# Kernel optimization log

Measured on AMD Instinct MI355X. Metric: run time of the kernel, lower is better.

The kernel has to match this reference:

```python
import jax, jax.numpy as jnp
import numpy as np

B = 131072      # batch size
ORDER = 8       # number of TT modes
N = 64          # grid points per mode (dims[i])
R = 32          # internal TT rank
EPS = 1e-8      # stability_eps
INIT_SCALE = 0.01


def setup_inputs() -> dict:
    key = jax.random.key(0)
    k_idx, k0, kmid, klast = jax.random.split(key, 4)
    indices = jax.random.randint(k_idx, (B, ORDER), 0, N, dtype=jnp.int64)
    # TT cores: core0 (1, N, R), middle cores (ORDER-2, R, N, R), core_last (R, N, 1)
    core0 = jax.random.normal(k0, (1, N, R), dtype=jnp.float32) * INIT_SCALE
    cores_mid = jax.random.normal(kmid, (ORDER - 2, R, N, R), dtype=jnp.float32) * INIT_SCALE
    core_last = jax.random.normal(klast, (R, N, 1), dtype=jnp.float32) * INIT_SCALE
    return {"indices": indices, "core0": core0, "cores_mid": cores_mid, "core_last": core_last}


def _tt_forward(indices, core0, cores_mid, core_last):
    order = 2 + cores_mid.shape[0]
    dims = jnp.array([core0.shape[1]] + [cores_mid.shape[2]] * cores_mid.shape[0]
                     + [core_last.shape[1]], dtype=indices.dtype)
    idx = jnp.clip(indices, 0, dims[None, :] - 1)

    # i == 0: core0[:, idx, :] -> [1, B, R] -> squeeze leading rank-1 -> [B, R]
    v = core0[0, idx[:, 0], :]

    def step(v, core, col_idx):
        sl = core[:, col_idx, :]                                  # [R, B, R']
        norm = jnp.linalg.norm(v, axis=1, keepdims=True) + EPS    # [B, 1]
        v_new = jnp.einsum('br,rbs->bs', v / norm, sl) * norm     # [B, R']
        return v_new

    # middle cores share shape -> scan over them (gather + normalized matvec chain)
    def scan_body(v, inputs):
        core, col = inputs
        return step(v, core, col), None

    mid_cols = idx[:, 1:order - 1].T  # [ORDER-2, B]
    v, _ = jax.lax.scan(scan_body, v, (cores_mid, mid_cols))

    # last core -> [B, 1] -> squeeze -> [B]
    v = step(v, core_last, idx[:, order - 1])
    return v[:, 0]


def reference(indices, core0, cores_mid, core_last):
    return _tt_forward(indices, core0, cores_mid, core_last)
```

## Files before the change

kernel.cpp:

```cpp
#include <hip/hip_runtime.h>
#include <hip/hip_fp16.h>


#define B_TOTAL 131072
#define NDIM 64
#define RANK 32
#define S_BLK 256
#define THREADS 256
#define VSTRIDE_H 40

typedef _Float16 half8 __attribute__((ext_vector_type(8)));
typedef _Float16 half4 __attribute__((ext_vector_type(4)));
typedef float    f32x4 __attribute__((ext_vector_type(4)));

__global__ __launch_bounds__(256) void build_tables(
    const float* __restrict__ core0, const float* __restrict__ mid,
    const float* __restrict__ lastc,
    half8* __restrict__ PKB, __half* __restrict__ T01, float* __restrict__ TL)
{
    const int id = blockIdx.x * 256 + threadIdx.x;
    if (id < 32768) {
        const int l  = id & 63;
        const int f  = (id >> 6) & 1;
        const int c  = (id >> 7) & 63;
        const int tt = id >> 13;
        const int q = l >> 4, li = l & 15;
        const int n = f * 16 + li;
        const int t = 1 + tt;
        half8 h;
        #pragma unroll
        for (int j = 0; j < 8; ++j) {
            const int k = q * 8 + j;
            h[j] = (_Float16)(16.0f * mid[((t * 32 + k) * 64 + c) * 32 + n]);
        }
        PKB[id] = h;
    } else if (id < 163840) {
        const int i2 = id - 32768;
        const int s = i2 & 31, c1 = (i2 >> 5) & 63, c0 = i2 >> 11;
        float acc = 0.f;
        #pragma unroll
        for (int r = 0; r < 32; ++r)
            acc = fmaf(core0[c0 * 32 + r], mid[(r * 64 + c1) * 32 + s], acc);
        T01[(c0 * 64 + c1) * 32 + s] = __float2half(acc * 256.0f);
    } else {
        const int i3 = id - 163840;
        const int c7 = i3 & 63, c6 = (i3 >> 6) & 63, r = i3 >> 12;
        const float* m5 = mid + 5 * 65536;
        float acc = 0.f;
        #pragma unroll
        for (int s = 0; s < 32; ++s)
            acc = fmaf(m5[(r * 64 + c6) * 32 + s], lastc[s * 64 + c7], acc);
        TL[(c6 * 64 + c7) * 32 + r] = acc * 256.0f;
    }
}

__global__ __launch_bounds__(256) void tt_main_t(
    const int* __restrict__ idx, const __half* __restrict__ T01,
    const half8* __restrict__ PKB, const float* __restrict__ TL,
    float* __restrict__ out)
{
    __shared__ __align__(16) __half vbuf[S_BLK * VSTRIDE_H];
    __shared__ unsigned short ord[4][S_BLK];
    __shared__ unsigned char  cols[S_BLK][8];
    __shared__ unsigned int   bases[4][65];
    __shared__ unsigned int   hist[4][64];

    const int tid  = threadIdx.x;
    const int lane = tid & 63;
    const int wv   = tid >> 6;
    const int li   = lane & 15;
    const int quad = lane >> 4;
    const int b0   = blockIdx.x * S_BLK;

    #pragma unroll
    for (int k = 0; k < S_BLK * 8; k += THREADS) {
        const int lin = k + tid;
        int v = idx[b0 * 8 + lin];
        v = min(max(v, 0), NDIM - 1);
        cols[lin >> 3][lin & 7] = (unsigned char)v;
    }
    hist[tid >> 6][tid & 63] = 0;
    __syncthreads();

    unsigned int key[4], rank[4];
    #pragma unroll
    for (int tt = 0; tt < 4; ++tt) {
        key[tt]  = cols[tid][2 + tt];
        rank[tt] = atomicAdd(&hist[tt][key[tt]], 1u);
    }
    __syncthreads();
    {
        const unsigned int v = hist[wv][lane];
        unsigned int inc = v;
        #pragma unroll
        for (int d = 1; d < 64; d <<= 1) {
            const unsigned int n = __shfl_up(inc, d);
            if (lane >= d) inc += n;
        }
        bases[wv][lane] = inc - v;
        if (lane == 63) bases[wv][64] = inc;
    }
    __syncthreads();
    #pragma unroll
    for (int tt = 0; tt < 4; ++tt)
        ord[tt][bases[tt][key[tt]] + rank[tt]] = (unsigned short)tid;
    __syncthreads();

    {
        const int g = tid & 7, gid = tid >> 3;
        #pragma unroll
        for (int it = 0; it < S_BLK / 32; ++it) {
            const int s = it * 32 + gid;
            const int c0 = cols[s][0], c1 = cols[s][1];
            const uint2 q = *reinterpret_cast<const uint2*>(
                T01 + (c0 * 64 + c1) * 32 + 4 * g);
            unsigned int* vp = reinterpret_cast<unsigned int*>(vbuf) + s * (VSTRIDE_H / 2);
            vp[2 * g]     = q.x;
            vp[2 * g + 1] = q.y;
        }
    }
    __syncthreads();

    for (int tt = 0; tt < 4; ++tt) {
        const int cbase = wv * 16;
        half8 A0 = PKB[((tt * 64 + cbase) * 2 + 0) * 64 + lane];
        half8 A1 = PKB[((tt * 64 + cbase) * 2 + 1) * 64 + lane];
        for (int ci = 0; ci < 16; ++ci) {
            const int c = cbase + ci;
            half8 nA0 = A0, nA1 = A1;
            if (ci < 15) {
                nA0 = PKB[((tt * 64 + c + 1) * 2 + 0) * 64 + lane];
                nA1 = PKB[((tt * 64 + c + 1) * 2 + 1) * 64 + lane];
            }
            const int start = (int)bases[tt][c];
            const int end   = (int)bases[tt][c + 1];
            for (int p = start; p < end; p += 16) {
                const int pos = min(p + li, end - 1);
                const int sm  = (int)ord[tt][pos];
                const half8 Bv = *reinterpret_cast<const half8*>(
                    reinterpret_cast<const char*>(vbuf) + sm * 80 + quad * 16);
                f32x4 d0 = {0.f, 0.f, 0.f, 0.f}, d1 = {0.f, 0.f, 0.f, 0.f};
                d0 = __builtin_amdgcn_mfma_f32_16x16x32_f16(A0, Bv, d0, 0, 0, 0);
                d1 = __builtin_amdgcn_mfma_f32_16x16x32_f16(A1, Bv, d1, 0, 0, 0);
                half4 w0, w1;
                #pragma unroll
                for (int r = 0; r < 4; ++r) {
                    w0[r] = (_Float16)d0[r];
                    w1[r] = (_Float16)d1[r];
                }
                char* base = reinterpret_cast<char*>(vbuf) + sm * 80 + quad * 8;
                *reinterpret_cast<half4*>(base)      = w0;
                *reinterpret_cast<half4*>(base + 32) = w1;
            }
            A0 = nA0; A1 = nA1;
        }
        __syncthreads();
    }

    {
        const int g = tid & 7, gid = tid >> 3;
        #pragma unroll
        for (int it = 0; it < S_BLK / 32; ++it) {
            const int s = it * 32 + gid;
            const int c6 = cols[s][6], c7 = cols[s][7];
            const unsigned int* vp =
                reinterpret_cast<const unsigned int*>(vbuf) + s * (VSTRIDE_H / 2);
            const __half2 v01 = *reinterpret_cast<const __half2*>(&vp[2 * g]);
            const __half2 v23 = *reinterpret_cast<const __half2*>(&vp[2 * g + 1]);
            const float4 L = *reinterpret_cast<const float4*>(
                TL + (c6 * 64 + c7) * 32 + 4 * g);
            float o = 0.f;
            o = fmaf(__low2float(v01),  L.x, o);
            o = fmaf(__high2float(v01), L.y, o);
            o = fmaf(__low2float(v23),  L.z, o);
            o = fmaf(__high2float(v23), L.w, o);
            o += __shfl_xor(o, 1);
            o += __shfl_xor(o, 2);
            o += __shfl_xor(o, 4);
            if (g == 0) out[b0 + s] = o * 2.3283064365386963e-10f;
        }
    }
}

#define PKB_OFF 0u
#define TL_OFF  524288u
#define T01_OFF 1048576u

extern "C" void kernel_launch(void* const* d_in, const int* in_sizes, int n_in,
                              void* d_out, int out_size, void* d_ws, size_t ws_size,
                              hipStream_t stream) {
    const int*   idx   = (const int*)d_in[0];
    const float* core0 = (const float*)d_in[1];
    const float* mid   = (const float*)d_in[2];
    const float* lastc = (const float*)d_in[3];
    float* out = (float*)d_out;

    half8*  PKB = (half8*)((char*)d_ws + PKB_OFF);
    float*  TL  = (float*)((char*)d_ws + TL_OFF);
    __half* T01 = (__half*)((char*)d_ws + T01_OFF);

    hipLaunchKernelGGL(build_tables, dim3(294912 / 256), dim3(256), 0, stream,
                       core0, mid, lastc, PKB, T01, TL);
    hipLaunchKernelGGL(tt_main_t, dim3(B_TOTAL / S_BLK), dim3(THREADS), 0, stream,
                       idx, T01, PKB, TL, out);
}
```

Measured before the change: 84.21 us.

## Load-balance MFMA batches across waves via shared descriptor list with prefetch

```diff
diff --git a/kernel.cpp b/kernel.cpp
--- a/kernel.cpp
+++ b/kernel.cpp
@@ -8,6 +8,7 @@
 #define S_BLK 256
 #define THREADS 256
 #define VSTRIDE_H 40
+#define MAXB 80
 
 typedef _Float16 half8 __attribute__((ext_vector_type(8)));
 typedef _Float16 half4 __attribute__((ext_vector_type(4)));
@@ -54,7 +55,7 @@
     }
 }
 
-__global__ __launch_bounds__(256) void tt_main_t(
+__global__ __launch_bounds__(256) void tt_main_p(
     const int* __restrict__ idx, const __half* __restrict__ T01,
     const half8* __restrict__ PKB, const float* __restrict__ TL,
     float* __restrict__ out)
@@ -64,6 +65,8 @@
     __shared__ unsigned char  cols[S_BLK][8];
     __shared__ unsigned int   bases[4][65];
     __shared__ unsigned int   hist[4][64];
+    __shared__ unsigned int   desc[4][MAXB];
+    __shared__ unsigned int   nb[4];
 
     const int tid  = threadIdx.x;
     const int lane = tid & 63;
@@ -80,6 +83,7 @@
         cols[lin >> 3][lin & 7] = (unsigned char)v;
     }
     hist[tid >> 6][tid & 63] = 0;
+    if (tid < 4) nb[tid] = 0;
     __syncthreads();
 
     unsigned int key[4], rank[4];
@@ -104,6 +108,15 @@
     #pragma unroll
     for (int tt = 0; tt < 4; ++tt)
         ord[tt][bases[tt][key[tt]] + rank[tt]] = (unsigned short)tid;
+    {
+        const int tts = tid >> 6, c = tid & 63;
+        const int st = (int)bases[tts][c], en = (int)bases[tts][c + 1];
+        for (int p = st; p < en; p += 16) {
+            const unsigned int ln = (unsigned int)min(16, en - p);
+            const unsigned int slot = atomicAdd(&nb[tts], 1u);
+            desc[tts][slot] = (unsigned int)c | ((unsigned int)p << 6) | (ln << 15);
+        }
+    }
     __syncthreads();
 
     {
@@ -122,37 +135,47 @@
     __syncthreads();
 
     for (int tt = 0; tt < 4; ++tt) {
-        const int cbase = wv * 16;
-        half8 A0 = PKB[((tt * 64 + cbase) * 2 + 0) * 64 + lane];
-        half8 A1 = PKB[((tt * 64 + cbase) * 2 + 1) * 64 + lane];
-        for (int ci = 0; ci < 16; ++ci) {
-            const int c = cbase + ci;
-            half8 nA0 = A0, nA1 = A1;
-            if (ci < 15) {
-                nA0 = PKB[((tt * 64 + c + 1) * 2 + 0) * 64 + lane];
-                nA1 = PKB[((tt * 64 + c + 1) * 2 + 1) * 64 + lane];
+        const int n = (int)nb[tt];
+        int i = wv;
+        int sm = 0;
+        half8 A0 = {0,0,0,0,0,0,0,0}, A1 = {0,0,0,0,0,0,0,0};
+        half8 Bv = {0,0,0,0,0,0,0,0};
+        if (i < n) {
+            const unsigned int d = desc[tt][i];
+            const int c = d & 63, st = (d >> 6) & 511, ln = (d >> 15) & 31;
+            sm = (int)ord[tt][min(st + li, st + ln - 1)];
+            A0 = PKB[((tt * 64 + c) * 2 + 0) * 64 + lane];
+            A1 = PKB[((tt * 64 + c) * 2 + 1) * 64 + lane];
+            Bv = *reinterpret_cast<const half8*>(
+                reinterpret_cast<const char*>(vbuf) + sm * 80 + quad * 16);
+        }
+        while (i < n) {
+            const int inx = i + 4;
+            int smn = 0;
+            half8 A0n = {0,0,0,0,0,0,0,0}, A1n = {0,0,0,0,0,0,0,0};
+            half8 Bvn = {0,0,0,0,0,0,0,0};
+            if (inx < n) {
+                const unsigned int d = desc[tt][inx];
+                const int c = d & 63, st = (d >> 6) & 511, ln = (d >> 15) & 31;
+                smn = (int)ord[tt][min(st + li, st + ln - 1)];
+                A0n = PKB[((tt * 64 + c) * 2 + 0) * 64 + lane];
+                A1n = PKB[((tt * 64 + c) * 2 + 1) * 64 + lane];
+                Bvn = *reinterpret_cast<const half8*>(
+                    reinterpret_cast<const char*>(vbuf) + smn * 80 + quad * 16);
             }
-            const int start = (int)bases[tt][c];
-            const int end   = (int)bases[tt][c + 1];
-            for (int p = start; p < end; p += 16) {
-                const int pos = min(p + li, end - 1);
-                const int sm  = (int)ord[tt][pos];
-                const half8 Bv = *reinterpret_cast<const half8*>(
-                    reinterpret_cast<const char*>(vbuf) + sm * 80 + quad * 16);
-                f32x4 d0 = {0.f, 0.f, 0.f, 0.f}, d1 = {0.f, 0.f, 0.f, 0.f};
-                d0 = __builtin_amdgcn_mfma_f32_16x16x32_f16(A0, Bv, d0, 0, 0, 0);
-                d1 = __builtin_amdgcn_mfma_f32_16x16x32_f16(A1, Bv, d1, 0, 0, 0);
-                half4 w0, w1;
-                #pragma unroll
-                for (int r = 0; r < 4; ++r) {
-                    w0[r] = (_Float16)d0[r];
-                    w1[r] = (_Float16)d1[r];
-                }
-                char* base = reinterpret_cast<char*>(vbuf) + sm * 80 + quad * 8;
-                *reinterpret_cast<half4*>(base)      = w0;
-                *reinterpret_cast<half4*>(base + 32) = w1;
+            f32x4 d0 = {0.f, 0.f, 0.f, 0.f}, d1 = {0.f, 0.f, 0.f, 0.f};
+            d0 = __builtin_amdgcn_mfma_f32_16x16x32_f16(A0, Bv, d0, 0, 0, 0);
+            d1 = __builtin_amdgcn_mfma_f32_16x16x32_f16(A1, Bv, d1, 0, 0, 0);
+            half4 w0, w1;
+            #pragma unroll
+            for (int r = 0; r < 4; ++r) {
+                w0[r] = (_Float16)d0[r];
+                w1[r] = (_Float16)d1[r];
             }
-            A0 = nA0; A1 = nA1;
+            char* base = reinterpret_cast<char*>(vbuf) + sm * 80 + quad * 8;
+            *reinterpret_cast<half4*>(base)      = w0;
+            *reinterpret_cast<half4*>(base + 32) = w1;
+            i = inx; sm = smn; A0 = A0n; A1 = A1n; Bv = Bvn;
         }
         __syncthreads();
     }
@@ -201,6 +224,6 @@
 
     hipLaunchKernelGGL(build_tables, dim3(294912 / 256), dim3(256), 0, stream,
                        core0, mid, lastc, PKB, T01, TL);
-    hipLaunchKernelGGL(tt_main_t, dim3(B_TOTAL / S_BLK), dim3(THREADS), 0, stream,
+    hipLaunchKernelGGL(tt_main_p, dim3(B_TOTAL / S_BLK), dim3(THREADS), 0, stream,
                        idx, T01, PKB, TL, out);
 }
```

Measured after the change: 93.27 us. +10.8%, slower.

## Store vectors in sorted order with ping-pong buffers and software-pipelined column groups

Applied to the files above, without the earlier changes.

```diff
diff --git a/kernel.cpp b/kernel.cpp
--- a/kernel.cpp
+++ b/kernel.cpp
@@ -4,10 +4,9 @@
 
 #define B_TOTAL 131072
 #define NDIM 64
-#define RANK 32
 #define S_BLK 256
 #define THREADS 256
-#define VSTRIDE_H 40
+#define VSH 40
 
 typedef _Float16 half8 __attribute__((ext_vector_type(8)));
 typedef _Float16 half4 __attribute__((ext_vector_type(4)));
@@ -54,16 +53,17 @@
     }
 }
 
-__global__ __launch_bounds__(256) void tt_main_t(
+__global__ __launch_bounds__(256) void tt_main_s(
     const int* __restrict__ idx, const __half* __restrict__ T01,
     const half8* __restrict__ PKB, const float* __restrict__ TL,
     float* __restrict__ out)
 {
-    __shared__ __align__(16) __half vbuf[S_BLK * VSTRIDE_H];
-    __shared__ unsigned short ord[4][S_BLK];
+    __shared__ __align__(16) __half vbuf2[2][S_BLK * VSH];
     __shared__ unsigned char  cols[S_BLK][8];
     __shared__ unsigned int   bases[4][65];
     __shared__ unsigned int   hist[4][64];
+    __shared__ unsigned short nxt[4][S_BLK];
+    __shared__ unsigned short pos0[S_BLK];
 
     const int tid  = threadIdx.x;
     const int lane = tid & 63;
@@ -101,9 +101,15 @@
         if (lane == 63) bases[wv][64] = inc;
     }
     __syncthreads();
-    #pragma unroll
-    for (int tt = 0; tt < 4; ++tt)
-        ord[tt][bases[tt][key[tt]] + rank[tt]] = (unsigned short)tid;
+    {
+        unsigned int p[4];
+        #pragma unroll
+        for (int tt = 0; tt < 4; ++tt) p[tt] = bases[tt][key[tt]] + rank[tt];
+        pos0[tid] = (unsigned short)p[0];
+        #pragma unroll
+        for (int tt = 0; tt < 3; ++tt) nxt[tt][p[tt]] = (unsigned short)p[tt + 1];
+        nxt[3][p[3]] = (unsigned short)tid;
+    }
     __syncthreads();
 
     {
@@ -114,7 +120,8 @@
             const int c0 = cols[s][0], c1 = cols[s][1];
             const uint2 q = *reinterpret_cast<const uint2*>(
                 T01 + (c0 * 64 + c1) * 32 + 4 * g);
-            unsigned int* vp = reinterpret_cast<unsigned int*>(vbuf) + s * (VSTRIDE_H / 2);
+            const int ps = (int)pos0[s];
+            unsigned int* vp = reinterpret_cast<unsigned int*>(&vbuf2[0][ps * VSH]);
             vp[2 * g]     = q.x;
             vp[2 * g + 1] = q.y;
         }
@@ -122,37 +129,73 @@
     __syncthreads();
 
     for (int tt = 0; tt < 4; ++tt) {
+        const __half* src = vbuf2[tt & 1];
+        __half*       dst = vbuf2[(tt + 1) & 1];
         const int cbase = wv * 16;
-        half8 A0 = PKB[((tt * 64 + cbase) * 2 + 0) * 64 + lane];
-        half8 A1 = PKB[((tt * 64 + cbase) * 2 + 1) * 64 + lane];
+        const int bval = (int)bases[tt][cbase + (lane < 17 ? lane : 16)];
+
+        int   stp[2], enp[2], wpp[2];
+        half8 Afp[2][2], Bvp[2];
+        #pragma unroll
+        for (int j = 0; j < 2; ++j) {
+            const int st = __shfl(bval, j);
+            const int en = __shfl(bval, j + 1);
+            const int c  = cbase + j;
+            stp[j] = st; enp[j] = en;
+            Afp[j][0] = PKB[((tt * 64 + c) * 2 + 0) * 64 + lane];
+            Afp[j][1] = PKB[((tt * 64 + c) * 2 + 1) * 64 + lane];
+            int pp = min(st + li, max(en - 1, st)); pp = min(pp, S_BLK - 1);
+            wpp[j] = (int)nxt[tt][pp];
+            Bvp[j] = *reinterpret_cast<const half8*>(&src[pp * VSH + quad * 8]);
+        }
+        #pragma unroll
         for (int ci = 0; ci < 16; ++ci) {
-            const int c = cbase + ci;
-            half8 nA0 = A0, nA1 = A1;
-            if (ci < 15) {
-                nA0 = PKB[((tt * 64 + c + 1) * 2 + 0) * 64 + lane];
-                nA1 = PKB[((tt * 64 + c + 1) * 2 + 1) * 64 + lane];
-            }
-            const int start = (int)bases[tt][c];
-            const int end   = (int)bases[tt][c + 1];
-            for (int p = start; p < end; p += 16) {
-                const int pos = min(p + li, end - 1);
-                const int sm  = (int)ord[tt][pos];
-                const half8 Bv = *reinterpret_cast<const half8*>(
-                    reinterpret_cast<const char*>(vbuf) + sm * 80 + quad * 16);
+            const int cur = ci & 1;
+            const int st = stp[cur], en = enp[cur];
+            if (st < en) {
                 f32x4 d0 = {0.f, 0.f, 0.f, 0.f}, d1 = {0.f, 0.f, 0.f, 0.f};
-                d0 = __builtin_amdgcn_mfma_f32_16x16x32_f16(A0, Bv, d0, 0, 0, 0);
-                d1 = __builtin_amdgcn_mfma_f32_16x16x32_f16(A1, Bv, d1, 0, 0, 0);
+                d0 = __builtin_amdgcn_mfma_f32_16x16x32_f16(Afp[cur][0], Bvp[cur], d0, 0, 0, 0);
+                d1 = __builtin_amdgcn_mfma_f32_16x16x32_f16(Afp[cur][1], Bvp[cur], d1, 0, 0, 0);
                 half4 w0, w1;
                 #pragma unroll
                 for (int r = 0; r < 4; ++r) {
                     w0[r] = (_Float16)d0[r];
                     w1[r] = (_Float16)d1[r];
                 }
-                char* base = reinterpret_cast<char*>(vbuf) + sm * 80 + quad * 8;
+                __half* base = &dst[wpp[cur] * VSH + quad * 4];
                 *reinterpret_cast<half4*>(base)      = w0;
-                *reinterpret_cast<half4*>(base + 32) = w1;
+                *reinterpret_cast<half4*>(base + 16) = w1;
+                for (int p = st + 16; p < en; p += 16) {
+                    const int pp2 = min(p + li, en - 1);
+                    const half8 Bx = *reinterpret_cast<const half8*>(
+                        &src[pp2 * VSH + quad * 8]);
+                    const int wx = (int)nxt[tt][pp2];
+                    f32x4 e0 = {0.f, 0.f, 0.f, 0.f}, e1 = {0.f, 0.f, 0.f, 0.f};
+                    e0 = __builtin_amdgcn_mfma_f32_16x16x32_f16(Afp[cur][0], Bx, e0, 0, 0, 0);
+                    e1 = __builtin_amdgcn_mfma_f32_16x16x32_f16(Afp[cur][1], Bx, e1, 0, 0, 0);
+                    half4 x0, x1;
+                    #pragma unroll
+                    for (int r = 0; r < 4; ++r) {
+                        x0[r] = (_Float16)e0[r];
+                        x1[r] = (_Float16)e1[r];
+                    }
+                    __half* bb = &dst[wx * VSH + quad * 4];
+                    *reinterpret_cast<half4*>(bb)      = x0;
+                    *reinterpret_cast<half4*>(bb + 16) = x1;
+                }
             }
-            A0 = nA0; A1 = nA1;
+            if (ci + 2 < 16) {
+                const int j  = ci + 2;
+                const int st2 = __shfl(bval, j);
+                const int en2 = __shfl(bval, j + 1);
+                const int c2  = cbase + j;
+                stp[cur] = st2; enp[cur] = en2;
+                Afp[cur][0] = PKB[((tt * 64 + c2) * 2 + 0) * 64 + lane];
+                Afp[cur][1] = PKB[((tt * 64 + c2) * 2 + 1) * 64 + lane];
+                int pp = min(st2 + li, max(en2 - 1, st2)); pp = min(pp, S_BLK - 1);
+                wpp[cur] = (int)nxt[tt][pp];
+                Bvp[cur] = *reinterpret_cast<const half8*>(&src[pp * VSH + quad * 8]);
+            }
         }
         __syncthreads();
     }
@@ -164,7 +207,7 @@
             const int s = it * 32 + gid;
             const int c6 = cols[s][6], c7 = cols[s][7];
             const unsigned int* vp =
-                reinterpret_cast<const unsigned int*>(vbuf) + s * (VSTRIDE_H / 2);
+                reinterpret_cast<const unsigned int*>(&vbuf2[0][s * VSH]);
             const __half2 v01 = *reinterpret_cast<const __half2*>(&vp[2 * g]);
             const __half2 v23 = *reinterpret_cast<const __half2*>(&vp[2 * g + 1]);
             const float4 L = *reinterpret_cast<const float4*>(
@@ -201,6 +244,6 @@
 
     hipLaunchKernelGGL(build_tables, dim3(294912 / 256), dim3(256), 0, stream,
                        core0, mid, lastc, PKB, T01, TL);
-    hipLaunchKernelGGL(tt_main_t, dim3(B_TOTAL / S_BLK), dim3(THREADS), 0, stream,
+    hipLaunchKernelGGL(tt_main_s, dim3(B_TOTAL / S_BLK), dim3(THREADS), 0, stream,
                        idx, T01, PKB, TL, out);
 }
```

Result: no change. 83.95 us (-0.3%).

## Template main kernel on block size and launch 1024-sample blocks

Applied to the files above, without the earlier changes.

```diff
diff --git a/kernel.cpp b/kernel.cpp
--- a/kernel.cpp
+++ b/kernel.cpp
@@ -4,10 +4,6 @@
 
 #define B_TOTAL 131072
 #define NDIM 64
-#define RANK 32
-#define S_BLK 256
-#define THREADS 256
-#define VSTRIDE_H 40
 
 typedef _Float16 half8 __attribute__((ext_vector_type(8)));
 typedef _Float16 half4 __attribute__((ext_vector_type(4)));
@@ -54,67 +50,74 @@
     }
 }
 
-__global__ __launch_bounds__(256) void tt_main_t(
+template<int SBLK>
+__global__ __launch_bounds__(SBLK) void tt_main_v(
     const int* __restrict__ idx, const __half* __restrict__ T01,
     const half8* __restrict__ PKB, const float* __restrict__ TL,
     float* __restrict__ out)
 {
-    __shared__ __align__(16) __half vbuf[S_BLK * VSTRIDE_H];
-    __shared__ unsigned short ord[4][S_BLK];
-    __shared__ unsigned char  cols[S_BLK][8];
-    __shared__ unsigned int   bases[4][65];
-    __shared__ unsigned int   hist[4][64];
+    constexpr int NW  = SBLK / 64;
+    constexpr int CPW = 64 / NW;
+    extern __shared__ __align__(16) char smem[];
+    __half*         vbuf  = reinterpret_cast<__half*>(smem);
+    unsigned short* ord   = reinterpret_cast<unsigned short*>(smem + SBLK * 80);
+    unsigned int*   cols2 = reinterpret_cast<unsigned int*>(smem + SBLK * 88);
+    unsigned int*   hist  = reinterpret_cast<unsigned int*>(smem + SBLK * 92);
+    unsigned int*   bases = hist + 256;
 
     const int tid  = threadIdx.x;
     const int lane = tid & 63;
     const int wv   = tid >> 6;
     const int li   = lane & 15;
     const int quad = lane >> 4;
-    const int b0   = blockIdx.x * S_BLK;
-
+    const int b0   = blockIdx.x * SBLK;
+
+    const int4* idx4 = reinterpret_cast<const int4*>(idx) + (size_t)(b0 + tid) * 2;
+    const int4 ia = idx4[0], ib = idx4[1];
+    const int c0 = min(max(ia.x, 0), 63), c1 = min(max(ia.y, 0), 63);
+    int key[4];
+    key[0] = min(max(ia.z, 0), 63);
+    key[1] = min(max(ia.w, 0), 63);
+    key[2] = min(max(ib.x, 0), 63);
+    key[3] = min(max(ib.y, 0), 63);
+    const int c6 = min(max(ib.z, 0), 63), c7 = min(max(ib.w, 0), 63);
+    cols2[tid] = (unsigned)c0 | ((unsigned)c1 << 8) |
+                 ((unsigned)c6 << 16) | ((unsigned)c7 << 24);
+    if (tid < 256) hist[tid] = 0;
+    __syncthreads();
+
+    unsigned int rank[4];
     #pragma unroll
-    for (int k = 0; k < S_BLK * 8; k += THREADS) {
-        const int lin = k + tid;
-        int v = idx[b0 * 8 + lin];
-        v = min(max(v, 0), NDIM - 1);
-        cols[lin >> 3][lin & 7] = (unsigned char)v;
-    }
-    hist[tid >> 6][tid & 63] = 0;
-    __syncthreads();
-
-    unsigned int key[4], rank[4];
-    #pragma unroll
-    for (int tt = 0; tt < 4; ++tt) {
-        key[tt]  = cols[tid][2 + tt];
-        rank[tt] = atomicAdd(&hist[tt][key[tt]], 1u);
-    }
-    __syncthreads();
-    {
-        const unsigned int v = hist[wv][lane];
+    for (int tt = 0; tt < 4; ++tt)
+        rank[tt] = atomicAdd(&hist[tt * 64 + key[tt]], 1u);
+    __syncthreads();
+    if (wv < 4) {
+        const unsigned int v = hist[wv * 64 + lane];
         unsigned int inc = v;
         #pragma unroll
         for (int d = 1; d < 64; d <<= 1) {
             const unsigned int n = __shfl_up(inc, d);
             if (lane >= d) inc += n;
         }
-        bases[wv][lane] = inc - v;
-        if (lane == 63) bases[wv][64] = inc;
+        bases[wv * 65 + lane] = inc - v;
+        if (lane == 63) bases[wv * 65 + 64] = inc;
     }
     __syncthreads();
     #pragma unroll
     for (int tt = 0; tt < 4; ++tt)
-        ord[tt][bases[tt][key[tt]] + rank[tt]] = (unsigned short)tid;
-    __syncthreads();
-
+        ord[tt * SBLK + bases[tt * 65 + key[tt]] + rank[tt]] = (unsigned short)tid;
+
+    __syncthreads();
     {
         const int g = tid & 7, gid = tid >> 3;
         #pragma unroll
-        for (int it = 0; it < S_BLK / 32; ++it) {
-            const int s = it * 32 + gid;
-            const int c0 = cols[s][0], c1 = cols[s][1];
+        for (int it = 0; it < 8; ++it) {
+            const int s = it * (SBLK / 8) + gid;
+            const unsigned cc = cols2[s];
+            const int a = cc & 255, b = (cc >> 8) & 255;
             const uint2 q = *reinterpret_cast<const uint2*>(
-                T01 + (c0 * 64 + c1) * 32 + 4 * g);
-            unsigned int* vp = reinterpret_cast<unsigned int*>(vbuf) + s * (VSTRIDE_H / 2);
+                T01 + (a * 64 + b) * 32 + 4 * g);
+            unsigned int* vp = reinterpret_cast<unsigned int*>(vbuf + s * 40);
             vp[2 * g]     = q.x;
             vp[2 * g + 1] = q.y;
         }
@@ -122,23 +125,22 @@
     __syncthreads();
 
     for (int tt = 0; tt < 4; ++tt) {
-        const int cbase = wv * 16;
+        const int cbase = wv * CPW;
         half8 A0 = PKB[((tt * 64 + cbase) * 2 + 0) * 64 + lane];
         half8 A1 = PKB[((tt * 64 + cbase) * 2 + 1) * 64 + lane];
-        for (int ci = 0; ci < 16; ++ci) {
+        for (int ci = 0; ci < CPW; ++ci) {
             const int c = cbase + ci;
             half8 nA0 = A0, nA1 = A1;
-            if (ci < 15) {
+            if (ci + 1 < CPW) {
                 nA0 = PKB[((tt * 64 + c + 1) * 2 + 0) * 64 + lane];
                 nA1 = PKB[((tt * 64 + c + 1) * 2 + 1) * 64 + lane];
             }
-            const int start = (int)bases[tt][c];
-            const int end   = (int)bases[tt][c + 1];
-            for (int p = start; p < end; p += 16) {
-                const int pos = min(p + li, end - 1);
-                const int sm  = (int)ord[tt][pos];
+            const int st = (int)bases[tt * 65 + c];
+            const int en = (int)bases[tt * 65 + c + 1];
+            for (int p = st; p < en; p += 16) {
+                const int sm = (int)ord[tt * SBLK + min(p + li, en - 1)];
                 const half8 Bv = *reinterpret_cast<const half8*>(
-                    reinterpret_cast<const char*>(vbuf) + sm * 80 + quad * 16);
+                    vbuf + sm * 40 + quad * 8);
                 f32x4 d0 = {0.f, 0.f, 0.f, 0.f}, d1 = {0.f, 0.f, 0.f, 0.f};
                 d0 = __builtin_amdgcn_mfma_f32_16x16x32_f16(A0, Bv, d0, 0, 0, 0);
                 d1 = __builtin_amdgcn_mfma_f32_16x16x32_f16(A1, Bv, d1, 0, 0, 0);
@@ -148,9 +150,9 @@
                     w0[r] = (_Float16)d0[r];
                     w1[r] = (_Float16)d1[r];
                 }
-                char* base = reinterpret_cast<char*>(vbuf) + sm * 80 + quad * 8;
-                *reinterpret_cast<half4*>(base)      = w0;
-                *reinterpret_cast<half4*>(base + 32) = w1;
+                __half* basep = vbuf + sm * 40 + quad * 4;
+                *reinterpret_cast<half4*>(basep)      = w0;
+                *reinterpret_cast<half4*>(basep + 16) = w1;
             }
             A0 = nA0; A1 = nA1;
         }
@@ -160,15 +162,16 @@
     {
         const int g = tid & 7, gid = tid >> 3;
         #pragma unroll
-        for (int it = 0; it < S_BLK / 32; ++it) {
-            const int s = it * 32 + gid;
-            const int c6 = cols[s][6], c7 = cols[s][7];
+        for (int it = 0; it < 8; ++it) {
+            const int s = it * (SBLK / 8) + gid;
+            const unsigned cc = cols2[s];
+            const int a = (cc >> 16) & 255, b = cc >> 24;
             const unsigned int* vp =
-                reinterpret_cast<const unsigned int*>(vbuf) + s * (VSTRIDE_H / 2);
+                reinterpret_cast<const unsigned int*>(vbuf + s * 40);
             const __half2 v01 = *reinterpret_cast<const __half2*>(&vp[2 * g]);
             const __half2 v23 = *reinterpret_cast<const __half2*>(&vp[2 * g + 1]);
             const float4 L = *reinterpret_cast<const float4*>(
-                TL + (c6 * 64 + c7) * 32 + 4 * g);
+                TL + (a * 64 + b) * 32 + 4 * g);
             float o = 0.f;
             o = fmaf(__low2float(v01),  L.x, o);
             o = fmaf(__high2float(v01), L.y, o);
@@ -185,6 +188,7 @@
 #define PKB_OFF 0u
 #define TL_OFF  524288u
 #define T01_OFF 1048576u
+#define SMEM_BYTES(SBLK) ((SBLK) * 92 + 256 * 4 + 4 * 65 * 4)
 
 extern "C" void kernel_launch(void* const* d_in, const int* in_sizes, int n_in,
                               void* d_out, int out_size, void* d_ws, size_t ws_size,
@@ -201,6 +205,15 @@
 
     hipLaunchKernelGGL(build_tables, dim3(294912 / 256), dim3(256), 0, stream,
                        core0, mid, lastc, PKB, T01, TL);
-    hipLaunchKernelGGL(tt_main_t, dim3(B_TOTAL / S_BLK), dim3(THREADS), 0, stream,
-                       idx, T01, PKB, TL, out);
+
+    const hipError_t aerr = hipFuncSetAttribute(
+        reinterpret_cast<const void*>(&tt_main_v<1024>),
+        hipFuncAttributeMaxDynamicSharedMemorySize, SMEM_BYTES(1024));
+    if (aerr == hipSuccess) {
+        hipLaunchKernelGGL((tt_main_v<1024>), dim3(B_TOTAL / 1024), dim3(1024),
+                           SMEM_BYTES(1024), stream, idx, T01, PKB, TL, out);
+    } else {
+        hipLaunchKernelGGL((tt_main_v<512>), dim3(B_TOTAL / 512), dim3(512),
+                           SMEM_BYTES(512), stream, idx, T01, PKB, TL, out);
+    }
 }
```

New measurement: 82.02 us. 1.03x faster.
